# Performance work log

Hardware: AMD Instinct MI355X
Metric: run time of the kernel (lower is better)

The kernel has to match this reference:

```python
import jax, jax.numpy as jnp
import numpy as np

N_NODES = 50000
N_EDGES = 600000
IN_DIM = 128
HID = 128
N_CLASSES = 40
N_GRAPHS = 128


def setup_inputs() -> dict:
    key = jax.random.key(0)
    ks = jax.random.split(key, 12)
    x = jax.random.normal(ks[0], (N_NODES, IN_DIM), dtype=jnp.float32)
    edge_index = jax.random.randint(ks[1], (2, N_EDGES), 0, N_NODES, dtype=jnp.int64)
    batch = jnp.sort(jax.random.randint(ks[2], (N_NODES,), 0, N_GRAPHS, dtype=jnp.int64))
    dims = [IN_DIM, HID, HID, N_CLASSES]
    params = {}
    for l in range(3):
        d_in, d_out = dims[l], dims[l + 1]
        s = 1.0 / np.sqrt(d_in)
        params[f"Wl{l}"] = jax.random.uniform(ks[3 + 3 * l], (d_out, d_in), jnp.float32, -s, s)
        params[f"bl{l}"] = jax.random.uniform(ks[4 + 3 * l], (d_out,), jnp.float32, -s, s)
        params[f"Wr{l}"] = jax.random.uniform(ks[5 + 3 * l], (d_out, d_in), jnp.float32, -s, s)
    return {"x": x, "edge_index": edge_index, "batch": batch, **params}


def _sage_layer(h, src, dst, Wl, bl, Wr):
    # message: relu(x_j) (edge_attr is None -> zero), mean-aggregate at dst
    m = jnp.maximum(h[src], 0.0)                       # [E, d]
    agg = jax.ops.segment_sum(m, dst, num_segments=N_NODES)
    cnt = jax.ops.segment_sum(jnp.ones((m.shape[0],), h.dtype), dst, num_segments=N_NODES)
    agg = agg / jnp.maximum(cnt, 1.0)[:, None]
    # lin_l(agg) + lin_r(x)
    return agg @ Wl.T + bl + h @ Wr.T


def reference(x, edge_index, batch, Wl0, bl0, Wr0, Wl1, bl1, Wr1, Wl2, bl2, Wr2):
    src, dst = edge_index[0], edge_index[1]
    Ws = [(Wl0, bl0, Wr0), (Wl1, bl1, Wr1), (Wl2, bl2, Wr2)]
    h = x
    for l, (Wl, bl, Wr) in enumerate(Ws):
        # dropout is identity in eval mode
        h = _sage_layer(h, src, dst, Wl, bl, Wr)
        if l != len(Ws) - 1:
            h = jnp.maximum(h, 0.0)
    # global mean pool over graphs
    gsum = jax.ops.segment_sum(h, batch, num_segments=N_GRAPHS)
    gcnt = jax.ops.segment_sum(jnp.ones((h.shape[0],), h.dtype), batch, num_segments=N_GRAPHS)
    g = gsum / jnp.maximum(gcnt, 1.0)[:, None]
    return h, g
```

## Files before the change

### kernel.cpp

```cpp
#include <hip/hip_runtime.h>
#include <hip/hip_bf16.h>


#define NODES 50000
#define K_DIM 128
#define N_GRAPHS 128

typedef __attribute__((ext_vector_type(8))) short short8;
typedef __attribute__((ext_vector_type(4))) short short4v;
typedef __attribute__((ext_vector_type(4))) float f32x4;

__device__ inline short f2bf(float f) {
    unsigned u = __builtin_bit_cast(unsigned, f);
    u += 0x7FFFu + ((u >> 16) & 1u);
    return (short)(u >> 16);
}
__device__ inline float bf2f(short h) {
    unsigned u = ((unsigned)(unsigned short)h) << 16;
    return __builtin_bit_cast(float, u);
}
__device__ inline float blo(unsigned u) { return __builtin_bit_cast(float, u << 16); }
__device__ inline float bhi(unsigned u) { return __builtin_bit_cast(float, u & 0xFFFF0000u); }
__device__ inline unsigned hilo_pack(float f) {
    short h = f2bf(f);
    short l = f2bf(f - bf2f(h));
    return ((unsigned)(unsigned short)h) | (((unsigned)(unsigned short)l) << 16);
}

__global__ void init_kernel(const float* __restrict__ w0, const float* __restrict__ w1,
                            const float* __restrict__ w2, const float* __restrict__ w3,
                            const float* __restrict__ w4, const float* __restrict__ w5,
                            short* __restrict__ whi, short* __restrict__ wlo,
                            int* __restrict__ deg, const int* __restrict__ batch,
                            int* __restrict__ gstart, int* __restrict__ counter,
                            const float* __restrict__ x, short* __restrict__ xb,
                            float* __restrict__ gsum, int N) {
    int idx = blockIdx.x * 256 + threadIdx.x;
    if (idx < N * (K_DIM / 4)) {
        float4 v = reinterpret_cast<const float4*>(x)[idx];
        short4v b;
        b[0] = f2bf(fmaxf(v.x, 0.f));
        b[1] = f2bf(fmaxf(v.y, 0.f));
        b[2] = f2bf(fmaxf(v.z, 0.f));
        b[3] = f2bf(fmaxf(v.w, 0.f));
        *reinterpret_cast<short4v*>(&xb[idx * 4]) = b;
    }
    if (idx < N) deg[idx] = 0;
    if (idx < N_GRAPHS * 40) gsum[idx] = 0.f;
    if (idx == 0) *counter = 0;
    const int TOT = 4 * 16384 + 96 * 128;
    if (idx < TOT) {
        float v;
        if (idx < 65536) {
            int m = idx >> 14, e = idx & 16383;
            const float* W = (m == 0) ? w0 : (m == 1) ? w1 : (m == 2) ? w2 : w3;
            v = W[e];
        } else {
            int i2 = idx - 65536;
            int row = i2 >> 7, col = i2 & 127;
            if (row < 40)      v = w4[row * 128 + col];
            else if (row < 80) v = w5[(row - 40) * 128 + col];
            else               v = 0.f;
        }
        unsigned p = hilo_pack(v);
        whi[idx] = (short)(p & 0xFFFFu);
        wlo[idx] = (short)(p >> 16);
    }
    if (idx <= N_GRAPHS) {
        int g = idx;
        int lo = 0, hi = N;
        while (lo < hi) {
            int mid = (lo + hi) >> 1;
            if (batch[mid] < g) lo = mid + 1; else hi = mid;
        }
        gstart[g] = lo;
    }
}

__global__ void deg_kernel(const int* __restrict__ dst, int* __restrict__ deg, int E) {
    int e = blockIdx.x * blockDim.x + threadIdx.x;
    if (e < E) atomicAdd(&deg[dst[e]], 1);
}

__global__ void csr_offsets(const int* __restrict__ deg, int* __restrict__ counter,
                            int* __restrict__ rowptr, int* __restrict__ fillpos, int N) {
    const int tid = threadIdx.x, lane = tid & 63, wv = tid >> 6;
    int i = blockIdx.x * 256 + tid;
    int v = (i < N) ? deg[i] : 0;
    int incl = v;
    #pragma unroll
    for (int off = 1; off < 64; off <<= 1) {
        int t = __shfl_up(incl, off, 64);
        if (lane >= off) incl += t;
    }
    __shared__ int ws[4];
    __shared__ int sbase;
    if (lane == 63) ws[wv] = incl;
    __syncthreads();
    if (tid == 0) sbase = atomicAdd(counter, ws[0] + ws[1] + ws[2] + ws[3]);
    __syncthreads();
    int add = sbase;
    for (int k = 0; k < wv; ++k) add += ws[k];
    int excl = add + incl - v;
    if (i < N) { rowptr[i] = excl; fillpos[i] = excl; }
}

__global__ void fill_kernel(const int* __restrict__ src, const int* __restrict__ dst,
                            int* __restrict__ fillpos, int* __restrict__ csr_src, int E) {
    int e = blockIdx.x * blockDim.x + threadIdx.x;
    if (e < E) {
        int p = atomicAdd(&fillpos[dst[e]], 1);
        csr_src[p] = src[e];
    }
}

__global__ void agg_bf16(const unsigned short* __restrict__ hb,
                         const int* __restrict__ rowptr, const int* __restrict__ deg,
                         const int* __restrict__ csr_src,
                         short* __restrict__ aggb, int N) {
    int w = (blockIdx.x * blockDim.x + threadIdx.x) >> 6;
    if (w >= N) return;
    int lane = threadIdx.x & 63;
    int slot = lane >> 4, l16 = lane & 15;
    int s = rowptr[w];
    int e = s + deg[w];
    const uint4* T = reinterpret_cast<const uint4*>(hb);
    float2 a0 = make_float2(0.f, 0.f), a1 = a0, a2 = a0, a3 = a0;
    int i = s + slot;
    for (; i + 4 < e; i += 8) {
        uint4 va = T[(size_t)csr_src[i] * 16 + l16];
        uint4 vb = T[(size_t)csr_src[i + 4] * 16 + l16];
        a0.x += blo(va.x) + blo(vb.x); a0.y += bhi(va.x) + bhi(vb.x);
        a1.x += blo(va.y) + blo(vb.y); a1.y += bhi(va.y) + bhi(vb.y);
        a2.x += blo(va.z) + blo(vb.z); a2.y += bhi(va.z) + bhi(vb.z);
        a3.x += blo(va.w) + blo(vb.w); a3.y += bhi(va.w) + bhi(vb.w);
    }
    for (; i < e; i += 4) {
        uint4 va = T[(size_t)csr_src[i] * 16 + l16];
        a0.x += blo(va.x); a0.y += bhi(va.x);
        a1.x += blo(va.y); a1.y += bhi(va.y);
        a2.x += blo(va.z); a2.y += bhi(va.z);
        a3.x += blo(va.w); a3.y += bhi(va.w);
    }
    #pragma unroll
    for (int off = 16; off <= 32; off <<= 1) {
        a0.x += __shfl_xor(a0.x, off, 64); a0.y += __shfl_xor(a0.y, off, 64);
        a1.x += __shfl_xor(a1.x, off, 64); a1.y += __shfl_xor(a1.y, off, 64);
        a2.x += __shfl_xor(a2.x, off, 64); a2.y += __shfl_xor(a2.y, off, 64);
        a3.x += __shfl_xor(a3.x, off, 64); a3.y += __shfl_xor(a3.y, off, 64);
    }
    if (slot == 0) {
        float inv = 1.0f / fmaxf((float)(e - s), 1.0f);
        short8 b;
        b[0] = f2bf(a0.x * inv); b[1] = f2bf(a0.y * inv);
        b[2] = f2bf(a1.x * inv); b[3] = f2bf(a1.y * inv);
        b[4] = f2bf(a2.x * inv); b[5] = f2bf(a2.y * inv);
        b[6] = f2bf(a3.x * inv); b[7] = f2bf(a3.y * inv);
        *reinterpret_cast<short8*>(&aggb[(size_t)w * K_DIM + l16 * 8]) = b;
    }
}

template<bool XF32>
__global__ __launch_bounds__(256) void sage_mfma_t(
        const short* __restrict__ Ab_in,
        const short* __restrict__ Hhi_in, const short* __restrict__ Hlo_in,
        const float* __restrict__ Xf,
        const short* __restrict__ Bhl, const short* __restrict__ Bll,
        const short* __restrict__ Bhr, const short* __restrict__ Blr,
        const float* __restrict__ bl,
        short* __restrict__ outHi, short* __restrict__ outLo, int N) {
    constexpr int BM = 64;
    constexpr int LSTR = 40;
    const int tid = threadIdx.x;
    const int lane = tid & 63;
    const int wave = tid >> 6;
    const int l15 = lane & 15;
    const int quad = lane >> 4;
    const int m0 = blockIdx.x * BM;
    const int srow = tid >> 2, sc8 = tid & 3;

    __shared__ __align__(16) short Ab [BM * LSTR];
    __shared__ __align__(16) short Ahi[BM * LSTR];
    __shared__ __align__(16) short Alo[BM * LSTR];

    f32x4 acc[4][2];
    #pragma unroll
    for (int i = 0; i < 4; ++i)
        #pragma unroll
        for (int j = 0; j < 2; ++j) acc[i][j] = (f32x4){0.f, 0.f, 0.f, 0.f};

    const short8 zero8 = (short8){0, 0, 0, 0, 0, 0, 0, 0};
    const int sm = m0 + srow;

    for (int k0 = 0; k0 < K_DIM; k0 += 32) {
        __syncthreads();
        {
            short8 va = zero8, vh = zero8, vl = zero8;
            if (sm < N) {
                va = *reinterpret_cast<const short8*>(Ab_in + (size_t)sm * K_DIM + k0 + sc8 * 8);
                if constexpr (XF32) {
                    const float* xp = Xf + (size_t)sm * K_DIM + k0 + sc8 * 8;
                    float4 f0 = *reinterpret_cast<const float4*>(xp);
                    float4 f1 = *reinterpret_cast<const float4*>(xp + 4);
                    float fv[8] = {f0.x, f0.y, f0.z, f0.w, f1.x, f1.y, f1.z, f1.w};
                    #pragma unroll
                    for (int j = 0; j < 8; ++j) {
                        unsigned p = hilo_pack(fv[j]);
                        vh[j] = (short)(p & 0xFFFFu);
                        vl[j] = (short)(p >> 16);
                    }
                } else {
                    vh = *reinterpret_cast<const short8*>(Hhi_in + (size_t)sm * K_DIM + k0 + sc8 * 8);
                    vl = *reinterpret_cast<const short8*>(Hlo_in + (size_t)sm * K_DIM + k0 + sc8 * 8);
                }
            }
            *reinterpret_cast<short8*>(&Ab [srow * LSTR + sc8 * 8]) = va;
            *reinterpret_cast<short8*>(&Ahi[srow * LSTR + sc8 * 8]) = vh;
            *reinterpret_cast<short8*>(&Alo[srow * LSTR + sc8 * 8]) = vl;
        }
        short8 bhl_[2], bll_[2], bhr_[2], blr_[2];
        #pragma unroll
        for (int nt = 0; nt < 2; ++nt) {
            int n = wave * 32 + nt * 16 + l15;
            size_t off = (size_t)n * K_DIM + k0 + quad * 8;
            bhl_[nt] = *reinterpret_cast<const short8*>(Bhl + off);
            bll_[nt] = *reinterpret_cast<const short8*>(Bll + off);
            bhr_[nt] = *reinterpret_cast<const short8*>(Bhr + off);
            blr_[nt] = *reinterpret_cast<const short8*>(Blr + off);
        }
        __syncthreads();
        #pragma unroll
        for (int mt = 0; mt < 4; ++mt) {
            int row = mt * 16 + l15;
            short8 ab = *reinterpret_cast<const short8*>(&Ab [row * LSTR + quad * 8]);
            short8 ah = *reinterpret_cast<const short8*>(&Ahi[row * LSTR + quad * 8]);
            short8 ao = *reinterpret_cast<const short8*>(&Alo[row * LSTR + quad * 8]);
            #pragma unroll
            for (int nt = 0; nt < 2; ++nt) {
                acc[mt][nt] = __builtin_amdgcn_mfma_f32_16x16x32_bf16(ab, bhl_[nt], acc[mt][nt], 0, 0, 0);
                acc[mt][nt] = __builtin_amdgcn_mfma_f32_16x16x32_bf16(ab, bll_[nt], acc[mt][nt], 0, 0, 0);
                acc[mt][nt] = __builtin_amdgcn_mfma_f32_16x16x32_bf16(ah, bhr_[nt], acc[mt][nt], 0, 0, 0);
                acc[mt][nt] = __builtin_amdgcn_mfma_f32_16x16x32_bf16(ah, blr_[nt], acc[mt][nt], 0, 0, 0);
                acc[mt][nt] = __builtin_amdgcn_mfma_f32_16x16x32_bf16(ao, bhr_[nt], acc[mt][nt], 0, 0, 0);
            }
        }
    }

    #pragma unroll
    for (int mt = 0; mt < 4; ++mt) {
        #pragma unroll
        for (int nt = 0; nt < 2; ++nt) {
            int col = wave * 32 + nt * 16 + l15;
            float b = bl[col];
            #pragma unroll
            for (int reg = 0; reg < 4; ++reg) {
                int row = m0 + mt * 16 + quad * 4 + reg;
                if (row < N) {
                    float v = fmaxf(acc[mt][nt][reg] + b, 0.f);
                    unsigned p = hilo_pack(v);
                    outHi[(size_t)row * K_DIM + col] = (short)(p & 0xFFFFu);
                    outLo[(size_t)row * K_DIM + col] = (short)(p >> 16);
                }
            }
        }
    }
}

__global__ __launch_bounds__(256) void gemm80(
        const short* __restrict__ Xhi, const short* __restrict__ Xlo,
        const short* __restrict__ Bh, const short* __restrict__ Bv,
        const float* __restrict__ b2,
        short* __restrict__ ylb, float* __restrict__ yr40, int N) {
    constexpr int BM = 64;
    constexpr int LSTR = 40;
    const int tid = threadIdx.x;
    const int lane = tid & 63;
    const int wave = tid >> 6;
    const int wm = wave & 1;
    const int wn = wave >> 1;
    const int l15 = lane & 15;
    const int quad = lane >> 4;
    const int m0 = blockIdx.x * BM;
    const int srow = tid >> 2, sc8 = tid & 3;

    __shared__ __align__(16) short Ahi[BM * LSTR];
    __shared__ __align__(16) short Alo[BM * LSTR];

    f32x4 acc[2][3];
    #pragma unroll
    for (int i = 0; i < 2; ++i)
        #pragma unroll
        for (int j = 0; j < 3; ++j) acc[i][j] = (f32x4){0.f, 0.f, 0.f, 0.f};

    const short8 zero8 = (short8){0, 0, 0, 0, 0, 0, 0, 0};
    const int sm = m0 + srow;

    for (int k0 = 0; k0 < K_DIM; k0 += 32) {
        __syncthreads();
        {
            short8 vh = zero8, vl = zero8;
            if (sm < N) {
                vh = *reinterpret_cast<const short8*>(Xhi + (size_t)sm * K_DIM + k0 + sc8 * 8);
                vl = *reinterpret_cast<const short8*>(Xlo + (size_t)sm * K_DIM + k0 + sc8 * 8);
            }
            *reinterpret_cast<short8*>(&Ahi[srow * LSTR + sc8 * 8]) = vh;
            *reinterpret_cast<short8*>(&Alo[srow * LSTR + sc8 * 8]) = vl;
        }
        short8 bh[3], bo[3];
        #pragma unroll
        for (int nt = 0; nt < 3; ++nt) {
            int n = wn * 48 + nt * 16 + l15;
            bh[nt] = *reinterpret_cast<const short8*>(Bh + (size_t)n * K_DIM + k0 + quad * 8);
            bo[nt] = *reinterpret_cast<const short8*>(Bv + (size_t)n * K_DIM + k0 + quad * 8);
        }
        __syncthreads();
        #pragma unroll
        for (int mt = 0; mt < 2; ++mt) {
            int row = wm * 32 + mt * 16 + l15;
            short8 ah = *reinterpret_cast<const short8*>(&Ahi[row * LSTR + quad * 8]);
            short8 ao = *reinterpret_cast<const short8*>(&Alo[row * LSTR + quad * 8]);
            #pragma unroll
            for (int nt = 0; nt < 3; ++nt) {
                acc[mt][nt] = __builtin_amdgcn_mfma_f32_16x16x32_bf16(ah, bh[nt], acc[mt][nt], 0, 0, 0);
                acc[mt][nt] = __builtin_amdgcn_mfma_f32_16x16x32_bf16(ah, bo[nt], acc[mt][nt], 0, 0, 0);
                acc[mt][nt] = __builtin_amdgcn_mfma_f32_16x16x32_bf16(ao, bh[nt], acc[mt][nt], 0, 0, 0);
            }
        }
    }

    #pragma unroll
    for (int mt = 0; mt < 2; ++mt) {
        #pragma unroll
        for (int nt = 0; nt < 3; ++nt) {
            int col = wn * 48 + nt * 16 + l15;
            #pragma unroll
            for (int reg = 0; reg < 4; ++reg) {
                int row = m0 + wm * 32 + mt * 16 + quad * 4 + reg;
                if (row < N) {
                    float v = acc[mt][nt][reg];
                    if (col < 40) {
                        ylb[(size_t)row * 40 + col] = f2bf(v);
                    } else if (col < 80) {
                        yr40[(size_t)row * 40 + (col - 40)] = v + b2[col - 40];
                    }
                }
            }
        }
    }
}

__global__ __launch_bounds__(256) void agg40_pool(
        const unsigned int* __restrict__ ylbu, const float* __restrict__ yr40,
        const int* __restrict__ rowptr, const int* __restrict__ deg,
        const int* __restrict__ csr_src,
        const int* __restrict__ batch, const int* __restrict__ gstart,
        float* __restrict__ out, float* __restrict__ gsum, int N) {
    const int w = (blockIdx.x * blockDim.x + threadIdx.x) >> 6;
    const int lane = threadIdx.x & 63;
    const int wv = threadIdx.x >> 6;
    const int half = lane >> 5, l32 = lane & 31;
    __shared__ float sh[4][40];
    __shared__ int sg[4];
    __shared__ float sinv[4];

    if (w < N) {
        int s = rowptr[w], e = s + deg[w];
        float ax = 0.f, ay = 0.f;
        if (l32 < 20) {
            int i = s + half;
            for (; i + 6 < e; i += 8) {
                int s0 = csr_src[i], s1 = csr_src[i + 2], s2 = csr_src[i + 4], s3 = csr_src[i + 6];
                unsigned v0 = ylbu[(size_t)s0 * 20 + l32];
                unsigned v1 = ylbu[(size_t)s1 * 20 + l32];
                unsigned v2 = ylbu[(size_t)s2 * 20 + l32];
                unsigned v3 = ylbu[(size_t)s3 * 20 + l32];
                ax += (blo(v0) + blo(v1)) + (blo(v2) + blo(v3));
                ay += (bhi(v0) + bhi(v1)) + (bhi(v2) + bhi(v3));
            }
            for (; i < e; i += 2) {
                unsigned v0 = ylbu[(size_t)csr_src[i] * 20 + l32];
                ax += blo(v0); ay += bhi(v0);
            }
        }
        ax += __shfl_xor(ax, 32, 64);
        ay += __shfl_xor(ay, 32, 64);
        if (half == 0 && l32 < 20) {
            float inv = 1.0f / fmaxf((float)(e - s), 1.0f);
            float2 yr = *reinterpret_cast<const float2*>(&yr40[(size_t)w * 40 + 2 * l32]);
            float vx = ax * inv + yr.x;
            float vy = ay * inv + yr.y;
            *reinterpret_cast<float2*>(&out[(size_t)w * 40 + 2 * l32]) = make_float2(vx, vy);
            sh[wv][2 * l32]     = vx;
            sh[wv][2 * l32 + 1] = vy;
        }
    }
    if (lane == 0) {
        if (w < N) {
            int g = batch[w];
            sg[wv] = g;
            sinv[wv] = 1.0f / fmaxf((float)(gstart[g + 1] - gstart[g]), 1.0f);
        } else {
            sg[wv] = -1;
        }
    }
    __syncthreads();
    if (wv == 0 && lane < 40) {
        int cur = -1;
        float accum = 0.f;
        #pragma unroll
        for (int k = 0; k < 4; ++k) {
            int gk = sg[k];
            if (gk < 0) continue;
            float c = sh[k][lane] * sinv[k];
            if (gk == cur) {
                accum += c;
            } else {
                if (cur >= 0) atomicAdd(&gsum[cur * 40 + lane], accum);
                cur = gk;
                accum = c;
            }
        }
        if (cur >= 0) atomicAdd(&gsum[cur * 40 + lane], accum);
    }
}

extern "C" void kernel_launch(void* const* d_in, const int* in_sizes, int n_in,
                              void* d_out, int out_size, void* d_ws, size_t ws_size,
                              hipStream_t stream) {
    const float* x    = (const float*)d_in[0];
    const int*   ei   = (const int*)d_in[1];
    const int*   batch= (const int*)d_in[2];
    const float* Wl0  = (const float*)d_in[3];
    const float* bl0  = (const float*)d_in[4];
    const float* Wr0  = (const float*)d_in[5];
    const float* Wl1  = (const float*)d_in[6];
    const float* bl1  = (const float*)d_in[7];
    const float* Wr1  = (const float*)d_in[8];
    const float* Wl2  = (const float*)d_in[9];
    const float* bl2  = (const float*)d_in[10];
    const float* Wr2  = (const float*)d_in[11];

    const int N = in_sizes[0] / K_DIM;
    const int E = in_sizes[1] / 2;
    const int* src = ei;
    const int* dst = ei + E;

    float* out = (float*)d_out;
    float* gsum = out + (size_t)N * 40;

    char* w = (char*)d_ws;
    auto alloc = [&](size_t bytes) {
        char* p = w;
        w += (bytes + 255) & ~(size_t)255;
        return p;
    };
    const size_t PL = (size_t)N * K_DIM * 2;
    short* aggb  = (short*)alloc(PL);
    short* xb    = (short*)alloc(PL);
    short* h1hi  = (short*)alloc(PL);
    short* h1lo  = (short*)alloc(PL);
    short* h2hi  = (short*)alloc(PL);
    short* h2lo  = (short*)alloc(PL);
    short* ylb   = (short*)alloc((size_t)N * 40 * 2);
    float* yr40  = (float*)alloc((size_t)N * 40 * 4);
    int*   rowptr= (int*)alloc((size_t)(N + 1) * 4);
    int*   deg   = (int*)alloc((size_t)N * 4);
    int*   fillp = (int*)alloc((size_t)N * 4);
    int*   csr   = (int*)alloc((size_t)E * 4);
    int*   counter = (int*)alloc(256);
    int*   gstart= (int*)alloc((size_t)(N_GRAPHS + 1) * 4);
    short* whi   = (short*)alloc(77824 * 2);
    short* wlo   = (short*)alloc(77824 * 2);

    const int NB = (N + 255) / 256;
    const int initGrid = (N * (K_DIM / 4) + 255) / 256;

    init_kernel<<<initGrid, 256, 0, stream>>>(Wl0, Wr0, Wl1, Wr1, Wl2, Wr2,
                                              whi, wlo, deg, batch, gstart, counter,
                                              x, xb, gsum, N);
    deg_kernel<<<(E + 255) / 256, 256, 0, stream>>>(dst, deg, E);
    csr_offsets<<<NB, 256, 0, stream>>>(deg, counter, rowptr, fillp, N);
    fill_kernel<<<(E + 255) / 256, 256, 0, stream>>>(src, dst, fillp, csr, E);

    short* hWl0 = whi;          short* lWl0 = wlo;
    short* hWr0 = whi + 16384;  short* lWr0 = wlo + 16384;
    short* hWl1 = whi + 32768;  short* lWl1 = wlo + 32768;
    short* hWr1 = whi + 49152;  short* lWr1 = wlo + 49152;
    short* hW2  = whi + 65536;  short* lW2  = wlo + 65536;

    const int aggGrid  = (N * 64 + 255) / 256;
    const int gemmGrid = (N + 63) / 64;

    agg_bf16<<<aggGrid, 256, 0, stream>>>((const unsigned short*)xb, rowptr, deg, csr, aggb, N);
    sage_mfma_t<true><<<gemmGrid, 256, 0, stream>>>(
        aggb, nullptr, nullptr, x, hWl0, lWl0, hWr0, lWr0, bl0, h1hi, h1lo, N);
    agg_bf16<<<aggGrid, 256, 0, stream>>>((const unsigned short*)h1hi, rowptr, deg, csr, aggb, N);
    sage_mfma_t<false><<<gemmGrid, 256, 0, stream>>>(
        aggb, h1hi, h1lo, nullptr, hWl1, lWl1, hWr1, lWr1, bl1, h2hi, h2lo, N);
    gemm80<<<gemmGrid, 256, 0, stream>>>(h2hi, h2lo, hW2, lW2, bl2, ylb, yr40, N);
    agg40_pool<<<aggGrid, 256, 0, stream>>>((const unsigned int*)ylb, yr40,
                                            rowptr, deg, csr, batch, gstart, out, gsum, N);
}
```

Before: 325.0 us.

## Fuse layer-1 SAGE GEMM with layer-2 projection GEMM via shared memory

Merges the layer-1 SAGE MFMA kernel and the 80-column layer-2 projection GEMM into one kernel. The layer-1 output tile (hi/lo bf16 split) goes to LDS instead of global memory, and the second GEMM reads it from there. This drops the h2hi/h2lo global round trip and one launch. In exchange it uses more LDS per block (about 50KB), which may reduce occupancy, and each wave re-reads B2 weights from global.

Measured after the change: 319.6 us. Within noise of the previous version (-1.7%).

```diff
diff --git a/kernel.cpp b/kernel.cpp
--- a/kernel.cpp
+++ b/kernel.cpp
@@ -160,11 +160,8 @@
     }
 }
 
-template<bool XF32>
-__global__ __launch_bounds__(256) void sage_mfma_t(
-        const short* __restrict__ Ab_in,
-        const short* __restrict__ Hhi_in, const short* __restrict__ Hlo_in,
-        const float* __restrict__ Xf,
+__global__ __launch_bounds__(256) void sage0_mfma(
+        const short* __restrict__ Ab_in, const float* __restrict__ Xf,
         const short* __restrict__ Bhl, const short* __restrict__ Bll,
         const short* __restrict__ Bhr, const short* __restrict__ Blr,
         const float* __restrict__ bl,
@@ -198,20 +195,15 @@
             short8 va = zero8, vh = zero8, vl = zero8;
             if (sm < N) {
                 va = *reinterpret_cast<const short8*>(Ab_in + (size_t)sm * K_DIM + k0 + sc8 * 8);
-                if constexpr (XF32) {
-                    const float* xp = Xf + (size_t)sm * K_DIM + k0 + sc8 * 8;
-                    float4 f0 = *reinterpret_cast<const float4*>(xp);
-                    float4 f1 = *reinterpret_cast<const float4*>(xp + 4);
-                    float fv[8] = {f0.x, f0.y, f0.z, f0.w, f1.x, f1.y, f1.z, f1.w};
-                    #pragma unroll
-                    for (int j = 0; j < 8; ++j) {
-                        unsigned p = hilo_pack(fv[j]);
-                        vh[j] = (short)(p & 0xFFFFu);
-                        vl[j] = (short)(p >> 16);
-                    }
-                } else {
-                    vh = *reinterpret_cast<const short8*>(Hhi_in + (size_t)sm * K_DIM + k0 + sc8 * 8);
-                    vl = *reinterpret_cast<const short8*>(Hlo_in + (size_t)sm * K_DIM + k0 + sc8 * 8);
+                const float* xp = Xf + (size_t)sm * K_DIM + k0 + sc8 * 8;
+                float4 f0 = *reinterpret_cast<const float4*>(xp);
+                float4 f1 = *reinterpret_cast<const float4*>(xp + 4);
+                float fv[8] = {f0.x, f0.y, f0.z, f0.w, f1.x, f1.y, f1.z, f1.w};
+                #pragma unroll
+                for (int j = 0; j < 8; ++j) {
+                    unsigned p = hilo_pack(fv[j]);
+                    vh[j] = (short)(p & 0xFFFFu);
+                    vl[j] = (short)(p >> 16);
                 }
             }
             *reinterpret_cast<short8*>(&Ab [srow * LSTR + sc8 * 8]) = va;
@@ -266,31 +258,37 @@
     }
 }
 
-__global__ __launch_bounds__(256) void gemm80(
-        const short* __restrict__ Xhi, const short* __restrict__ Xlo,
-        const short* __restrict__ Bh, const short* __restrict__ Bv,
+__global__ __launch_bounds__(256) void sage1_gemm80(
+        const short* __restrict__ Ab_in,
+        const short* __restrict__ Hhi_in, const short* __restrict__ Hlo_in,
+        const short* __restrict__ Bhl, const short* __restrict__ Bll,
+        const short* __restrict__ Bhr, const short* __restrict__ Blr,
+        const float* __restrict__ bl,
+        const short* __restrict__ B2h, const short* __restrict__ B2l,
         const float* __restrict__ b2,
         short* __restrict__ ylb, float* __restrict__ yr40, int N) {
     constexpr int BM = 64;
     constexpr int LSTR = 40;
+    constexpr int LSTR2 = 136;
     const int tid = threadIdx.x;
     const int lane = tid & 63;
     const int wave = tid >> 6;
-    const int wm = wave & 1;
-    const int wn = wave >> 1;
     const int l15 = lane & 15;
     const int quad = lane >> 4;
     const int m0 = blockIdx.x * BM;
     const int srow = tid >> 2, sc8 = tid & 3;
 
+    __shared__ __align__(16) short Ab [BM * LSTR];
     __shared__ __align__(16) short Ahi[BM * LSTR];
     __shared__ __align__(16) short Alo[BM * LSTR];
-
-    f32x4 acc[2][3];
-    #pragma unroll
-    for (int i = 0; i < 2; ++i)
-        #pragma unroll
-        for (int j = 0; j < 3; ++j) acc[i][j] = (f32x4){0.f, 0.f, 0.f, 0.f};
+    __shared__ __align__(16) short H2h[BM * LSTR2];
+    __shared__ __align__(16) short H2l[BM * LSTR2];
+
+    f32x4 acc[4][2];
+    #pragma unroll
+    for (int i = 0; i < 4; ++i)
+        #pragma unroll
+        for (int j = 0; j < 2; ++j) acc[i][j] = (f32x4){0.f, 0.f, 0.f, 0.f};
 
     const short8 zero8 = (short8){0, 0, 0, 0, 0, 0, 0, 0};
     const int sm = m0 + srow;
@@ -298,51 +296,96 @@
     for (int k0 = 0; k0 < K_DIM; k0 += 32) {
         __syncthreads();
         {
-            short8 vh = zero8, vl = zero8;
+            short8 va = zero8, vh = zero8, vl = zero8;
             if (sm < N) {
-                vh = *reinterpret_cast<const short8*>(Xhi + (size_t)sm * K_DIM + k0 + sc8 * 8);
-                vl = *reinterpret_cast<const short8*>(Xlo + (size_t)sm * K_DIM + k0 + sc8 * 8);
-            }
+                va = *reinterpret_cast<const short8*>(Ab_in  + (size_t)sm * K_DIM + k0 + sc8 * 8);
+                vh = *reinterpret_cast<const short8*>(Hhi_in + (size_t)sm * K_DIM + k0 + sc8 * 8);
+                vl = *reinterpret_cast<const short8*>(Hlo_in + (size_t)sm * K_DIM + k0 + sc8 * 8);
+            }
+            *reinterpret_cast<short8*>(&Ab [srow * LSTR + sc8 * 8]) = va;
             *reinterpret_cast<short8*>(&Ahi[srow * LSTR + sc8 * 8]) = vh;
             *reinterpret_cast<short8*>(&Alo[srow * LSTR + sc8 * 8]) = vl;
         }
-        short8 bh[3], bo[3];
-        #pragma unroll
-        for (int nt = 0; nt < 3; ++nt) {
-            int n = wn * 48 + nt * 16 + l15;
-            bh[nt] = *reinterpret_cast<const short8*>(Bh + (size_t)n * K_DIM + k0 + quad * 8);
-            bo[nt] = *reinterpret_cast<const short8*>(Bv + (size_t)n * K_DIM + k0 + quad * 8);
+        short8 bhl_[2], bll_[2], bhr_[2], blr_[2];
+        #pragma unroll
+        for (int nt = 0; nt < 2; ++nt) {
+            int n = wave * 32 + nt * 16 + l15;
+            size_t off = (size_t)n * K_DIM + k0 + quad * 8;
+            bhl_[nt] = *reinterpret_cast<const short8*>(Bhl + off);
+            bll_[nt] = *reinterpret_cast<const short8*>(Bll + off);
+            bhr_[nt] = *reinterpret_cast<const short8*>(Bhr + off);
+            blr_[nt] = *reinterpret_cast<const short8*>(Blr + off);
         }
         __syncthreads();
         #pragma unroll
-        for (int mt = 0; mt < 2; ++mt) {
-            int row = wm * 32 + mt * 16 + l15;
+        for (int mt = 0; mt < 4; ++mt) {
+            int row = mt * 16 + l15;
+            short8 ab = *reinterpret_cast<const short8*>(&Ab [row * LSTR + quad * 8]);
             short8 ah = *reinterpret_cast<const short8*>(&Ahi[row * LSTR + quad * 8]);
             short8 ao = *reinterpret_cast<const short8*>(&Alo[row * LSTR + quad * 8]);
             #pragma unroll
-            for (int nt = 0; nt < 3; ++nt) {
-                acc[mt][nt] = __builtin_amdgcn_mfma_f32_16x16x32_bf16(ah, bh[nt], acc[mt][nt], 0, 0, 0);
-                acc[mt][nt] = __builtin_amdgcn_mfma_f32_16x16x32_bf16(ah, bo[nt], acc[mt][nt], 0, 0, 0);
-                acc[mt][nt] = __builtin_amdgcn_mfma_f32_16x16x32_bf16(ao, bh[nt], acc[mt][nt], 0, 0, 0);
-            }
-        }
-    }
-
-    #pragma unroll
-    for (int mt = 0; mt < 2; ++mt) {
-        #pragma unroll
-        for (int nt = 0; nt < 3; ++nt) {
-            int col = wn * 48 + nt * 16 + l15;
+            for (int nt = 0; nt < 2; ++nt) {
+                acc[mt][nt] = __builtin_amdgcn_mfma_f32_16x16x32_bf16(ab, bhl_[nt], acc[mt][nt], 0, 0, 0);
+                acc[mt][nt] = __builtin_amdgcn_mfma_f32_16x16x32_bf16(ab, bll_[nt], acc[mt][nt], 0, 0, 0);
+                acc[mt][nt] = __builtin_amdgcn_mfma_f32_16x16x32_bf16(ah, bhr_[nt], acc[mt][nt], 0, 0, 0);
+                acc[mt][nt] = __builtin_amdgcn_mfma_f32_16x16x32_bf16(ah, blr_[nt], acc[mt][nt], 0, 0, 0);
+                acc[mt][nt] = __builtin_amdgcn_mfma_f32_16x16x32_bf16(ao, bhr_[nt], acc[mt][nt], 0, 0, 0);
+            }
+        }
+    }
+
+    __syncthreads();
+    #pragma unroll
+    for (int mt = 0; mt < 4; ++mt) {
+        #pragma unroll
+        for (int nt = 0; nt < 2; ++nt) {
+            int col = wave * 32 + nt * 16 + l15;
+            float b = bl[col];
             #pragma unroll
             for (int reg = 0; reg < 4; ++reg) {
-                int row = m0 + wm * 32 + mt * 16 + quad * 4 + reg;
-                if (row < N) {
-                    float v = acc[mt][nt][reg];
-                    if (col < 40) {
-                        ylb[(size_t)row * 40 + col] = f2bf(v);
-                    } else if (col < 80) {
-                        yr40[(size_t)row * 40 + (col - 40)] = v + b2[col - 40];
-                    }
+                int row = mt * 16 + quad * 4 + reg;
+                float v = fmaxf(acc[mt][nt][reg] + b, 0.f);
+                unsigned p = hilo_pack(v);
+                H2h[row * LSTR2 + col] = (short)(p & 0xFFFFu);
+                H2l[row * LSTR2 + col] = (short)(p >> 16);
+            }
+        }
+    }
+    __syncthreads();
+
+    f32x4 c2[5];
+    #pragma unroll
+    for (int nt = 0; nt < 5; ++nt) c2[nt] = (f32x4){0.f, 0.f, 0.f, 0.f};
+    const int arow = wave * 16 + l15;
+    #pragma unroll
+    for (int kc = 0; kc < 4; ++kc) {
+        const int k0 = kc * 32;
+        short8 ah = *reinterpret_cast<const short8*>(&H2h[arow * LSTR2 + k0 + quad * 8]);
+        short8 ao = *reinterpret_cast<const short8*>(&H2l[arow * LSTR2 + k0 + quad * 8]);
+        #pragma unroll
+        for (int nt = 0; nt < 5; ++nt) {
+            int n = nt * 16 + l15;
+            size_t off = (size_t)n * K_DIM + k0 + quad * 8;
+            short8 bh = *reinterpret_cast<const short8*>(B2h + off);
+            short8 bo = *reinterpret_cast<const short8*>(B2l + off);
+            c2[nt] = __builtin_amdgcn_mfma_f32_16x16x32_bf16(ah, bh, c2[nt], 0, 0, 0);
+            c2[nt] = __builtin_amdgcn_mfma_f32_16x16x32_bf16(ah, bo, c2[nt], 0, 0, 0);
+            c2[nt] = __builtin_amdgcn_mfma_f32_16x16x32_bf16(ao, bh, c2[nt], 0, 0, 0);
+        }
+    }
+
+    #pragma unroll
+    for (int nt = 0; nt < 5; ++nt) {
+        int col = nt * 16 + l15;
+        #pragma unroll
+        for (int reg = 0; reg < 4; ++reg) {
+            int row = m0 + wave * 16 + quad * 4 + reg;
+            if (row < N) {
+                float v = c2[nt][reg];
+                if (col < 40) {
+                    ylb[(size_t)row * 40 + col] = f2bf(v);
+                } else {
+                    yr40[(size_t)row * 40 + (col - 40)] = v + b2[col - 40];
                 }
             }
         }
@@ -459,8 +502,6 @@
     short* xb    = (short*)alloc(PL);
     short* h1hi  = (short*)alloc(PL);
     short* h1lo  = (short*)alloc(PL);
-    short* h2hi  = (short*)alloc(PL);
-    short* h2lo  = (short*)alloc(PL);
     short* ylb   = (short*)alloc((size_t)N * 40 * 2);
     float* yr40  = (float*)alloc((size_t)N * 40 * 4);
     int*   rowptr= (int*)alloc((size_t)(N + 1) * 4);
@@ -492,12 +533,11 @@
     const int gemmGrid = (N + 63) / 64;
 
     agg_bf16<<<aggGrid, 256, 0, stream>>>((const unsigned short*)xb, rowptr, deg, csr, aggb, N);
-    sage_mfma_t<true><<<gemmGrid, 256, 0, stream>>>(
-        aggb, nullptr, nullptr, x, hWl0, lWl0, hWr0, lWr0, bl0, h1hi, h1lo, N);
+    sage0_mfma<<<gemmGrid, 256, 0, stream>>>(
+        aggb, x, hWl0, lWl0, hWr0, lWr0, bl0, h1hi, h1lo, N);
     agg_bf16<<<aggGrid, 256, 0, stream>>>((const unsigned short*)h1hi, rowptr, deg, csr, aggb, N);
-    sage_mfma_t<false><<<gemmGrid, 256, 0, stream>>>(
-        aggb, h1hi, h1lo, nullptr, hWl1, lWl1, hWr1, lWr1, bl1, h2hi, h2lo, N);
-    gemm80<<<gemmGrid, 256, 0, stream>>>(h2hi, h2lo, hW2, lW2, bl2, ylb, yr40, N);
+    sage1_gemm80<<<gemmGrid, 256, 0, stream>>>(
+        aggb, h1hi, h1lo, hWl1, lWl1, hWr1, lWr1, bl1, hW2, lW2, bl2, ylb, yr40, N);
     agg40_pool<<<aggGrid, 256, 0, stream>>>((const unsigned int*)ylb, yr40,
                                             rowptr, deg, csr, batch, gstart, out, gsum, N);
 }
```
